# Performance work log

Measured on AMD Instinct MI355X. Metric: run time of the kernel, lower is better.

Reference implementation:

```python
import jax, jax.numpy as jnp
import numpy as np

N, E, D_IN, H, OUT = 50000, 800000, 128, 256, 2
BN_EPS = 1e-5
LN_EPS = 1e-5


def _xavier(k, fi, fo):
    lim = float(np.sqrt(6.0 / (fi + fo)))
    return jax.random.uniform(k, (fi, fo), minval=-lim, maxval=lim, dtype=jnp.float32)


def setup_inputs() -> dict:
    key = jax.random.key(0)
    ks = jax.random.split(key, 8)
    return {
        "x": jax.random.normal(ks[0], (N, D_IN), dtype=jnp.float32),
        "edge_index": jax.random.randint(ks[1], (2, E), 0, N, dtype=jnp.int32),
        "feature_scale": jnp.ones((D_IN,), jnp.float32),
        "feature_bias": jnp.zeros((D_IN,), jnp.float32),
        "bn0_g": jnp.ones((D_IN,), jnp.float32),
        "bn0_b": jnp.zeros((D_IN,), jnp.float32),
        "W1": _xavier(ks[2], D_IN, H), "b1": jnp.zeros((H,), jnp.float32),
        "bn1_g": jnp.ones((H,), jnp.float32), "bn1_b": jnp.zeros((H,), jnp.float32),
        "ln1_g": jnp.ones((H,), jnp.float32), "ln1_b": jnp.zeros((H,), jnp.float32),
        "W2": _xavier(ks[3], H, H), "b2": jnp.zeros((H,), jnp.float32),
        "bn2_g": jnp.ones((H,), jnp.float32), "bn2_b": jnp.zeros((H,), jnp.float32),
        "ln2_g": jnp.ones((H,), jnp.float32), "ln2_b": jnp.zeros((H,), jnp.float32),
        "Wout": _xavier(ks[4], H, OUT), "bout": jnp.zeros((OUT,), jnp.float32),
    }


def _batchnorm(x, g, b):
    # training-mode BatchNorm1d: batch stats over node axis, biased variance
    mu = jnp.mean(x, axis=0)
    var = jnp.mean(jnp.square(x - mu), axis=0)
    return g * (x - mu) * jax.lax.rsqrt(var + BN_EPS) + b


def _layernorm(x, g, b):
    mu = jnp.mean(x, axis=-1, keepdims=True)
    var = jnp.mean(jnp.square(x - mu), axis=-1, keepdims=True)
    return g * (x - mu) * jax.lax.rsqrt(var + LN_EPS) + b


def _gcn(x, W, b, src, dst, dinv):
    # PyG GCNConv with self-loops: D^{-1/2}(A+I)D^{-1/2} X W + b
    h = x @ W                                   # [N, F]
    norm = (dinv[src] * dinv[dst])[:, None]     # [E, 1]
    msg = h[src] * norm                         # [E, F] (dominant traffic)
    agg = jax.ops.segment_sum(msg, dst, num_segments=N)
    return agg + (dinv * dinv)[:, None] * h + b


def _forward(x, feature_scale, feature_bias, bn0_g, bn0_b,
             W1, b1, bn1_g, bn1_b, ln1_g, ln1_b,
             W2, b2, bn2_g, bn2_b, ln2_g, ln2_b,
             Wout, bout, edge_index):
    src, dst = edge_index[0], edge_index[1]
    deg = jax.ops.segment_sum(jnp.ones((E,), x.dtype), dst, num_segments=N) + 1.0
    dinv = jax.lax.rsqrt(deg)

    h = x * feature_scale + feature_bias
    h = _batchnorm(h, bn0_g, bn0_b)            # input_bn; dropout = identity (eval)

    # layer 0 (no residual: i == 0)
    h1 = _gcn(h, W1, b1, src, dst, dinv)
    h1 = jax.nn.relu(h1)
    h1 = _batchnorm(h1, bn1_g, bn1_b)
    h1 = _layernorm(h1, ln1_g, ln1_b)

    # layer 1 (residual add, shapes match)
    h2 = _gcn(h1, W2, b2, src, dst, dinv)
    h2 = jax.nn.relu(h2)
    h2 = _batchnorm(h2, bn2_g, bn2_b)
    h2 = _layernorm(h2, ln2_g, ln2_b)
    h2 = h2 + h1

    return h2 @ Wout + bout


def reference(x, edge_index, feature_scale, feature_bias, bn0_g, bn0_b,
              W1, b1, bn1_g, bn1_b, ln1_g, ln1_b,
              W2, b2, bn2_g, bn2_b, ln2_g, ln2_b,
              Wout, bout):
    return _forward(x, feature_scale, feature_bias, bn0_g, bn0_b,
                    W1, b1, bn1_g, bn1_b, ln1_g, ln1_b,
                    W2, b2, bn2_g, bn2_b, ln2_g, ln2_b,
                    Wout, bout, edge_index)
```

## Files before the change

kernel.cpp:

```cpp
#include <hip/hip_runtime.h>
#include <hip/hip_bf16.h>
#include <stdint.h>

#define N_NODES 50000
#define N_EDGES 800000
#define D_IN    128
#define H_DIM   256
#define BN_EPS  1e-5f
#define LN_EPS  1e-5f
#define NBLK2 782
#define SLICE_ELEMS ((size_t)N_NODES * 32)
#define EDGE_CHUNK 4096
#define BN0_BLOCKS 256
#define PREPX_BLOCKS 6250
#define TR_BLOCKS 256
#define NBKT 196
#define CHUNK 2048
#define RCHUNKS 391

typedef float v4f __attribute__((ext_vector_type(4)));
typedef float v2f __attribute__((ext_vector_type(2)));
typedef short v8s __attribute__((ext_vector_type(8)));
typedef unsigned v4u __attribute__((ext_vector_type(4)));

__device__ __forceinline__ float bflo(unsigned u){ return __uint_as_float(u << 16); }
__device__ __forceinline__ float bfhi(unsigned u){ return __uint_as_float(u & 0xffff0000u); }
__device__ __forceinline__ unsigned short f2bf(float f){
  unsigned u = __float_as_uint(f);
  u += 0x7fffu + ((u >> 16) & 1u);
  return (unsigned short)(u >> 16);
}
__device__ __forceinline__ unsigned pack2(float a, float b){
  return (unsigned)f2bf(a) | ((unsigned)f2bf(b) << 16);
}

__device__ __forceinline__ int block_excl_scan(int v){
  int t = threadIdx.x;
  int lane = t & 63, w = t >> 6;
  int inc = v;
  #pragma unroll
  for (int m = 1; m < 64; m <<= 1){
    int o = __shfl_up(inc, m, 64);
    if (lane >= m) inc += o;
  }
  __shared__ int wsum[4];
  if (lane == 63) wsum[w] = inc;
  __syncthreads();
  int base = 0;
  #pragma unroll
  for (int j = 0; j < 4; ++j) if (j < w) base += wsum[j];
  return base + inc - v;
}

__global__ __launch_bounds__(256) void bn0r1_k(const int* ei, const float* x,
                                               const float* fs, const float* fb,
                                               float* S, float* Q, int* ghist){
  int b = blockIdx.x, t = threadIdx.x;
  if (b >= BN0_BLOCKS){
    __shared__ int lh[NBKT];
    int b2 = b - BN0_BLOCKS;
    for (int i = t; i < NBKT; i += 256) lh[i] = 0;
    __syncthreads();
    int e0 = b2 * CHUNK;
    int n = min(CHUNK, N_EDGES - e0);
    for (int i = t; i < n; i += 256)
      atomicAdd(&lh[ei[N_EDGES + e0 + i] >> 8], 1);
    __syncthreads();
    if (t < NBKT && lh[t] > 0) atomicAdd(&ghist[t], lh[t]);
    return;
  }
  int cl = t & 31, rg = t >> 5;
  int c = cl * 4;
  float4 fs4 = *(const float4*)(fs + c);
  float4 fb4 = *(const float4*)(fb + c);
  float s0=0,s1=0,s2=0,s3=0,q0=0,q1=0,q2=0,q3=0;
  for (int row = b * 8 + rg; row < N_NODES; row += BN0_BLOCKS * 8){
    float4 xv = *(const float4*)(x + (size_t)row * D_IN + c);
    float v0 = xv.x * fs4.x + fb4.x;
    float v1 = xv.y * fs4.y + fb4.y;
    float v2 = xv.z * fs4.z + fb4.z;
    float v3 = xv.w * fs4.w + fb4.w;
    s0 += v0; s1 += v1; s2 += v2; s3 += v3;
    q0 += v0*v0; q1 += v1*v1; q2 += v2*v2; q3 += v3*v3;
  }
  __shared__ float red[256][8];
  red[t][0]=s0; red[t][1]=s1; red[t][2]=s2; red[t][3]=s3;
  red[t][4]=q0; red[t][5]=q1; red[t][6]=q2; red[t][7]=q3;
  __syncthreads();
  float* Sr = S + (b & 3) * D_IN;
  float* Qr = Q + (b & 3) * D_IN;
  if (t < 32){
    float a[8];
    #pragma unroll
    for (int i = 0; i < 8; ++i) a[i] = red[t][i];
    for (int j = 1; j < 8; ++j)
      #pragma unroll
      for (int i = 0; i < 8; ++i) a[i] += red[t + 32*j][i];
    #pragma unroll
    for (int i = 0; i < 4; ++i){ atomicAdd(&Sr[t*4+i], a[i]); atomicAdd(&Qr[t*4+i], a[4+i]); }
  }
}

__global__ __launch_bounds__(256) void r3_k(const int* ei, const int* ghist, int* gcursor, unsigned* ebuf){
  __shared__ unsigned short dstS[CHUNK];
  __shared__ int lh[NBKT], cb[NBKT], sbb[NBKT];
  int t = threadIdx.x;
  int v = (t < NBKT) ? ghist[t] : 0;
  int epre = block_excl_scan(v);
  if (t < NBKT){ sbb[t] = epre; lh[t] = 0; }
  __syncthreads();
  int e0 = blockIdx.x * CHUNK;
  int n = min(CHUNK, N_EDGES - e0);
  for (int i = t; i < n; i += 256){
    int d = ei[N_EDGES + e0 + i];
    dstS[i] = (unsigned short)d;
    atomicAdd(&lh[d >> 8], 1);
  }
  __syncthreads();
  if (t < NBKT && lh[t] > 0) cb[t] = sbb[t] + atomicAdd(&gcursor[t], lh[t]);
  __syncthreads();
  if (t < NBKT) lh[t] = 0;
  __syncthreads();
  for (int i = t; i < n; i += 256){
    int d = dstS[i];
    int bkt = d >> 8;
    int r = atomicAdd(&lh[bkt], 1);
    unsigned src = (unsigned)ei[e0 + i];
    ebuf[cb[bkt] + r] = ((unsigned)(d & 255) << 16) | src;
  }
}

__global__ __launch_bounds__(256) void dloc_k(const unsigned* ebuf, const int* ghist,
                                              int* perm, int* rank, int* offs, float* dinv){
  __shared__ int h[256], dh[128], ep_s[128], W_s[128], lc[128], sbb[NBKT + 1];
  int t = threadIdx.x, b = blockIdx.x;
  int gv = (t < NBKT) ? ghist[t] : 0;
  int gpre = block_excl_scan(gv);
  if (t < NBKT) sbb[t] = gpre;
  if (t == NBKT - 1) sbb[NBKT] = gpre + gv;
  h[t] = 0;
  if (t < 128){ dh[t] = 0; lc[t] = 0; }
  __syncthreads();
  int lo = sbb[b], hi = sbb[b + 1];
  for (int i = lo + t; i < hi; i += 256)
    atomicAdd(&h[(ebuf[i] >> 16) & 255], 1);
  __syncthreads();
  int node = b * 256 + t;
  bool valid = node < N_NODES;
  int deg = valid ? h[t] : 0;
  if (valid) atomicAdd(&dh[min(deg, 127)], 1);
  __syncthreads();
  int cv = (t < 128) ? dh[t] : 0;
  int e1 = block_excl_scan(cv);
  __syncthreads();
  int e2 = block_excl_scan((t < 128) ? cv * t : 0);
  __syncthreads();
  if (t < 128){ ep_s[t] = e1; W_s[t] = e2; }
  __syncthreads();
  if (valid){
    int bin = min(deg, 127);
    int r = atomicAdd(&lc[bin], 1);
    int pl = ep_s[bin] + r;
    int pos = b * 256 + pl;
    perm[pos] = node;
    rank[node] = pos;
    offs[pos] = lo + W_s[bin] + (pl - ep_s[bin]) * deg;
    dinv[node] = rsqrtf((float)deg + 1.0f);
  }
  if (b == 0 && t == 0) offs[N_NODES] = N_EDGES;
}

__global__ __launch_bounds__(256) void r4bprep_k(const unsigned* ebuf, const int* ghist,
                                                 const int* rank, const int* offs,
                                                 unsigned short* edges,
                                                 const float* x, const float* S, const float* Q,
                                                 const float* fs, const float* fb,
                                                 const float* gg, const float* bb,
                                                 unsigned short* xt,
                                                 const float* W1, const float* W2,
                                                 unsigned short* W1t, unsigned short* W2t){
  __shared__ int curs[256], sbb[NBKT + 1];
  int b = blockIdx.x, t = threadIdx.x;
  if (b < NBKT){
    int v = (t < NBKT) ? ghist[t] : 0;
    int epre = block_excl_scan(v);
    if (t < NBKT) sbb[t] = epre;
    if (t == NBKT - 1) sbb[NBKT] = epre + v;
    int node = b * 256 + t;
    if (node < N_NODES) curs[t] = offs[rank[node]];
    __syncthreads();
    int lo = sbb[b], hi = sbb[b + 1];
    for (int i = lo + t; i < hi; i += 256){
      unsigned u = ebuf[i];
      int l8 = (u >> 16) & 255;
      int pos = atomicAdd(&curs[l8], 1);
      edges[pos] = (unsigned short)(u & 0xffffu);
    }
    return;
  }
  if (b < NBKT + PREPX_BLOCKS){
    int i = (b - NBKT) * 256 + t;
    int row = i >> 5; int c = (i & 31) * 4;
    float4 Sv = *(const float4*)(S + c);
    float4 Qv = *(const float4*)(Q + c);
    #pragma unroll
    for (int rep = 1; rep < 4; ++rep){
      float4 s2 = *(const float4*)(S + rep * D_IN + c);
      float4 q2 = *(const float4*)(Q + rep * D_IN + c);
      Sv.x += s2.x; Sv.y += s2.y; Sv.z += s2.z; Sv.w += s2.w;
      Qv.x += q2.x; Qv.y += q2.y; Qv.z += q2.z; Qv.w += q2.w;
    }
    float4 fs4 = *(const float4*)(fs + c);
    float4 fb4 = *(const float4*)(fb + c);
    float4 gg4 = *(const float4*)(gg + c);
    float4 bb4 = *(const float4*)(bb + c);
    const float invN = 1.0f / N_NODES;
    float mu0 = Sv.x*invN, mu1 = Sv.y*invN, mu2 = Sv.z*invN, mu3 = Sv.w*invN;
    float r0 = rsqrtf(Qv.x*invN - mu0*mu0 + BN_EPS);
    float r1 = rsqrtf(Qv.y*invN - mu1*mu1 + BN_EPS);
    float r2 = rsqrtf(Qv.z*invN - mu2*mu2 + BN_EPS);
    float r3 = rsqrtf(Qv.w*invN - mu3*mu3 + BN_EPS);
    float a0 = gg4.x*r0*fs4.x, c0 = gg4.x*r0*(fb4.x - mu0) + bb4.x;
    float a1 = gg4.y*r1*fs4.y, c1 = gg4.y*r1*(fb4.y - mu1) + bb4.y;
    float a2 = gg4.z*r2*fs4.z, c2 = gg4.z*r2*(fb4.z - mu2) + bb4.z;
    float a3 = gg4.w*r3*fs4.w, c3 = gg4.w*r3*(fb4.w - mu3) + bb4.w;
    float4 xv = *(const float4*)(x + (size_t)row * D_IN + c);
    uint2 o;
    o.x = pack2(a0 * xv.x + c0, a1 * xv.y + c1);
    o.y = pack2(a2 * xv.z + c2, a3 * xv.w + c3);
    *(uint2*)(xt + (size_t)row * D_IN + c) = o;
    return;
  }
  int i = (b - NBKT - PREPX_BLOCKS) * 256 + t;
  if (i < D_IN * H_DIM){
    int r = i / H_DIM, c = i % H_DIM;
    W1t[c * D_IN + r] = f2bf(W1[i]);
  }
  if (i < H_DIM * H_DIM){
    int r = i / H_DIM, c = i % H_DIM;
    W2t[c * H_DIM + r] = f2bf(W2[i]);
  }
}

template<int K>
__global__ __launch_bounds__(256) void gemm_k(const unsigned short* A, const unsigned short* Bt,
                                              const float* dinv, unsigned short* C, int M){
  __shared__ __align__(16) short smem[16896];
  __shared__ float dvs[64];
  short* As = smem;
  short* Bs = smem + 64 * 40;
  int t = threadIdx.x;
  int m0 = blockIdx.x * 64;
  int lane = t & 63;
  int w = t >> 6;
  int fr = lane & 15, quad = lane >> 4;
  if (t < 64) dvs[t] = (m0 + t < M) ? dinv[m0 + t] : 0.0f;
  v4f acc[4][4] = {};
  int sr = t >> 2;
  int sk = (t & 3) << 3;
  for (int k0 = 0; k0 < K; k0 += 32){
    __syncthreads();
    uint4 av = {0,0,0,0};
    int arow = m0 + sr;
    if (arow < M) av = *(const uint4*)(A + (size_t)arow * K + k0 + sk);
    *(uint4*)(&As[sr * 40 + sk]) = av;
    #pragma unroll
    for (int j = 0; j < 4; ++j){
      int brow = sr + 64 * j;
      uint4 bv = *(const uint4*)(Bt + (size_t)brow * K + k0 + sk);
      *(uint4*)(&Bs[brow * 40 + sk]) = bv;
    }
    __syncthreads();
    v8s af[4], bf[4];
    #pragma unroll
    for (int mi = 0; mi < 4; ++mi)
      af[mi] = *(const v8s*)(&As[(mi * 16 + fr) * 40 + quad * 8]);
    #pragma unroll
    for (int ni = 0; ni < 4; ++ni)
      bf[ni] = *(const v8s*)(&Bs[(w * 64 + ni * 16 + fr) * 40 + quad * 8]);
    #pragma unroll
    for (int mi = 0; mi < 4; ++mi)
      #pragma unroll
      for (int ni = 0; ni < 4; ++ni)
        acc[mi][ni] = __builtin_amdgcn_mfma_f32_16x16x32_bf16(af[mi], bf[ni], acc[mi][ni], 0, 0, 0);
  }
  __syncthreads();
  short* Cs = smem;
  #pragma unroll
  for (int mi = 0; mi < 4; ++mi)
    #pragma unroll
    for (int ni = 0; ni < 4; ++ni)
      #pragma unroll
      for (int r = 0; r < 4; ++r){
        int row = mi * 16 + quad * 4 + r;
        int col = w * 64 + ni * 16 + fr;
        Cs[row * 264 + col] = (short)f2bf(acc[mi][ni][r] * dvs[row]);
      }
  __syncthreads();
  int orow = t >> 2;
  int grow = m0 + orow;
  if (grow < M){
    #pragma unroll
    for (int j = 0; j < 4; ++j){
      int oc = (t & 3) * 16 + 64 * j;
      v8s v0 = *(const v8s*)(&Cs[orow * 264 + oc]);
      v8s v1 = *(const v8s*)(&Cs[orow * 264 + oc + 8]);
      *(v8s*)(&C[(size_t)(oc >> 5) * SLICE_ELEMS + (size_t)grow * 32 + (oc & 31)]) = v0;
      int oc1 = oc + 8;
      *(v8s*)(&C[(size_t)(oc1 >> 5) * SLICE_ELEMS + (size_t)grow * 32 + (oc1 & 31)]) = v1;
    }
  }
}

#define ACCP(u, A) { v2f d_ = {bflo(u), bfhi(u)}; A += d_; }
#define ACC8(vv) ACCP(vv.x, A0) ACCP(vv.y, A1) ACCP(vv.z, A2) ACCP(vv.w, A3)

__global__ __launch_bounds__(256, 4) void agg_k(const unsigned short* hs, const int* offsets,
                                                const unsigned short* edges, const int* perm,
                                                const float* dinv, const float* bias,
                                                unsigned short* g, float* pS, float* pQ){
  __shared__ unsigned eds32[EDGE_CHUNK / 2];
  __shared__ float wps[4][4][16];
  int t = threadIdx.x;
  int lane = t & 63;
  int wv = t >> 6;
  int slice = blockIdx.x & 7;
  int l4 = lane & 3;
  int grp = blockIdx.x >> 3;
  int nb = grp * 64;
  int idx = nb + (t >> 2);
  int lastn = min(nb + 64, N_NODES);
  int blk0 = offsets[nb];
  int base = blk0 & ~1;
  int blkN = offsets[lastn];
  const unsigned* gsrc = (const unsigned*)(edges + base);
  int nu = min((blkN - base + 1) >> 1, EDGE_CHUNK / 2);
  for (int i = t; i < nu; i += 256)
    eds32[i] = gsrc[i];
  __syncthreads();
  bool act = idx < N_NODES;
  int node = act ? perm[idx] : 0;
  float dvv = act ? dinv[node] : 0.f;
  const uint4* hb4 = (const uint4*)(hs + (size_t)slice * SLICE_ELEMS);
  float4 bb0 = *(const float4*)(bias + slice * 32 + l4 * 8);
  float4 bb1 = *(const float4*)(bias + slice * 32 + l4 * 8 + 4);
  uint4 sv = hb4[(size_t)node * 4 + l4];
  v2f A0 = {bflo(sv.x), bfhi(sv.x)};
  v2f A1 = {bflo(sv.y), bfhi(sv.y)};
  v2f A2 = {bflo(sv.z), bfhi(sv.z)};
  v2f A3 = {bflo(sv.w), bfhi(sv.w)};
  int e  = act ? offsets[idx] : 0;
  int e1 = act ? offsets[idx + 1] : 0;
  if ((e & 1) && e < e1){
    int ru = (e - base) >> 1;
    unsigned d = (ru < EDGE_CHUNK / 2) ? eds32[ru] : gsrc[ru];
    uint4 vv = hb4[(size_t)(d >> 16) * 4 + l4];
    ACC8(vv);
    ++e;
  }
  for (; e + 16 <= e1; e += 16){
    int ru = (e - base) >> 1;
    unsigned dd[8];
    if (ru + 8 <= EDGE_CHUNK / 2){
      #pragma unroll
      for (int j = 0; j < 8; ++j) dd[j] = eds32[ru + j];
    } else {
      #pragma unroll
      for (int j = 0; j < 8; ++j) dd[j] = gsrc[ru + j];
    }
    uint4 v[16];
    #pragma unroll
    for (int j = 0; j < 8; ++j){
      v[2*j]   = hb4[(size_t)(dd[j] & 0xffffu) * 4 + l4];
      v[2*j+1] = hb4[(size_t)(dd[j] >> 16)     * 4 + l4];
    }
    #pragma unroll
    for (int j = 0; j < 16; ++j){ ACC8(v[j]); }
  }
  if (e + 8 <= e1){
    int ru = (e - base) >> 1;
    unsigned dd[4];
    if (ru + 4 <= EDGE_CHUNK / 2){
      #pragma unroll
      for (int j = 0; j < 4; ++j) dd[j] = eds32[ru + j];
    } else {
      #pragma unroll
      for (int j = 0; j < 4; ++j) dd[j] = gsrc[ru + j];
    }
    uint4 v[8];
    #pragma unroll
    for (int j = 0; j < 4; ++j){
      v[2*j]   = hb4[(size_t)(dd[j] & 0xffffu) * 4 + l4];
      v[2*j+1] = hb4[(size_t)(dd[j] >> 16)     * 4 + l4];
    }
    #pragma unroll
    for (int j = 0; j < 8; ++j){ ACC8(v[j]); }
    e += 8;
  }
  if (e + 4 <= e1){
    int ru = (e - base) >> 1;
    unsigned dd[2];
    if (ru + 2 <= EDGE_CHUNK / 2){
      dd[0] = eds32[ru]; dd[1] = eds32[ru + 1];
    } else {
      dd[0] = gsrc[ru]; dd[1] = gsrc[ru + 1];
    }
    uint4 v[4];
    #pragma unroll
    for (int j = 0; j < 2; ++j){
      v[2*j]   = hb4[(size_t)(dd[j] & 0xffffu) * 4 + l4];
      v[2*j+1] = hb4[(size_t)(dd[j] >> 16)     * 4 + l4];
    }
    #pragma unroll
    for (int j = 0; j < 4; ++j){ ACC8(v[j]); }
    e += 4;
  }
  for (; e < e1; ++e){
    int r = e - base;
    unsigned d = ((r >> 1) < EDGE_CHUNK / 2) ? eds32[r >> 1] : gsrc[r >> 1];
    unsigned s = (r & 1) ? (d >> 16) : (d & 0xffffu);
    uint4 vv = hb4[(size_t)s * 4 + l4];
    ACC8(vv);
  }
  float y0 = act ? fmaxf(dvv * A0.x + bb0.x, 0.f) : 0.f;
  float y1 = act ? fmaxf(dvv * A0.y + bb0.y, 0.f) : 0.f;
  float y2 = act ? fmaxf(dvv * A1.x + bb0.z, 0.f) : 0.f;
  float y3 = act ? fmaxf(dvv * A1.y + bb0.w, 0.f) : 0.f;
  float y4 = act ? fmaxf(dvv * A2.x + bb1.x, 0.f) : 0.f;
  float y5 = act ? fmaxf(dvv * A2.y + bb1.y, 0.f) : 0.f;
  float y6 = act ? fmaxf(dvv * A3.x + bb1.z, 0.f) : 0.f;
  float y7 = act ? fmaxf(dvv * A3.y + bb1.w, 0.f) : 0.f;
  if (act){
    v4u o;
    o.x = pack2(y0, y1); o.y = pack2(y2, y3);
    o.z = pack2(y4, y5); o.w = pack2(y6, y7);
    __builtin_nontemporal_store(o, (v4u*)(g + (size_t)node * H_DIM + slice * 32 + l4 * 8));
  }
  float q0 = y0*y0, q1 = y1*y1, q2 = y2*y2, q3 = y3*y3;
  float q4 = y4*y4, q5 = y5*y5, q6 = y6*y6, q7 = y7*y7;
  #pragma unroll
  for (int m = 4; m < 64; m <<= 1){
    y0 += __shfl_xor(y0, m, 64); y1 += __shfl_xor(y1, m, 64);
    y2 += __shfl_xor(y2, m, 64); y3 += __shfl_xor(y3, m, 64);
    y4 += __shfl_xor(y4, m, 64); y5 += __shfl_xor(y5, m, 64);
    y6 += __shfl_xor(y6, m, 64); y7 += __shfl_xor(y7, m, 64);
    q0 += __shfl_xor(q0, m, 64); q1 += __shfl_xor(q1, m, 64);
    q2 += __shfl_xor(q2, m, 64); q3 += __shfl_xor(q3, m, 64);
    q4 += __shfl_xor(q4, m, 64); q5 += __shfl_xor(q5, m, 64);
    q6 += __shfl_xor(q6, m, 64); q7 += __shfl_xor(q7, m, 64);
  }
  if (lane < 4){
    wps[wv][lane][0] = y0; wps[wv][lane][1] = y1; wps[wv][lane][2] = y2; wps[wv][lane][3] = y3;
    wps[wv][lane][4] = y4; wps[wv][lane][5] = y5; wps[wv][lane][6] = y6; wps[wv][lane][7] = y7;
    wps[wv][lane][8] = q0; wps[wv][lane][9] = q1; wps[wv][lane][10] = q2; wps[wv][lane][11] = q3;
    wps[wv][lane][12] = q4; wps[wv][lane][13] = q5; wps[wv][lane][14] = q6; wps[wv][lane][15] = q7;
  }
  __syncthreads();
  if (t < 64){
    int tl = t >> 4, ti = t & 15;
    float v = wps[0][tl][ti] + wps[1][tl][ti] + wps[2][tl][ti] + wps[3][tl][ti];
    int col32 = tl * 8 + (ti & 7);
    if (ti < 8) pS[(size_t)blockIdx.x * 32 + col32] = v;
    else        pQ[(size_t)blockIdx.x * 32 + col32] = v;
  }
}

__global__ __launch_bounds__(1024) void redu_k(const float* pS, const float* pQ,
                                               const float* gg, const float* bb,
                                               float* sc, float* sh){
  __shared__ float ls[32][32], lq[32][32];
  int t = threadIdx.x;
  int slice = blockIdx.x;
  int grp = t >> 5, c32 = t & 31;
  float as = 0.f, aq = 0.f;
  for (int blk2 = grp; blk2 < NBLK2; blk2 += 32){
    size_t o = ((size_t)blk2 * 8 + slice) * 32 + c32;
    as += pS[o]; aq += pQ[o];
  }
  ls[grp][c32] = as; lq[grp][c32] = aq;
  __syncthreads();
  if (t < 32){
    float S = 0.f, Q = 0.f;
    #pragma unroll
    for (int gI = 0; gI < 32; ++gI){ S += ls[gI][t]; Q += lq[gI][t]; }
    int col = slice * 32 + t;
    const float invN = 1.0f / N_NODES;
    float mu = S * invN;
    float rs = rsqrtf(Q * invN - mu * mu + BN_EPS);
    float s = gg[col] * rs;
    sc[col] = s;
    sh[col] = bb[col] - s * mu;
  }
}

__global__ __launch_bounds__(256) void apply1_k(const unsigned short* g, const float* sc, const float* sh,
                                                const float* lng, const float* lnb, unsigned short* h1){
  int t = threadIdx.x;
  int lane32 = t & 31;
  int row = blockIdx.x * 8 + (t >> 5);
  if (row >= N_NODES) return;
  int c = lane32 * 8;
  float4 s40 = *(const float4*)(sc + c);
  float4 s41 = *(const float4*)(sc + c + 4);
  float4 h40 = *(const float4*)(sh + c);
  float4 h41 = *(const float4*)(sh + c + 4);
  uint4 u = *(const uint4*)(g + (size_t)row * H_DIM + c);
  float v0 = s40.x * bflo(u.x) + h40.x;
  float v1 = s40.y * bfhi(u.x) + h40.y;
  float v2 = s40.z * bflo(u.y) + h40.z;
  float v3 = s40.w * bfhi(u.y) + h40.w;
  float v4 = s41.x * bflo(u.z) + h41.x;
  float v5 = s41.y * bfhi(u.z) + h41.y;
  float v6 = s41.z * bflo(u.w) + h41.z;
  float v7 = s41.w * bfhi(u.w) + h41.w;
  float sum = v0+v1+v2+v3+v4+v5+v6+v7;
  float sq  = v0*v0+v1*v1+v2*v2+v3*v3+v4*v4+v5*v5+v6*v6+v7*v7;
  #pragma unroll
  for (int m = 1; m < 32; m <<= 1){ sum += __shfl_xor(sum, m, 64); sq += __shfl_xor(sq, m, 64); }
  float mu = sum * (1.0f / H_DIM);
  float var = sq * (1.0f / H_DIM) - mu * mu;
  float rs = rsqrtf(var + LN_EPS);
  float4 g40 = *(const float4*)(lng + c);
  float4 g41 = *(const float4*)(lng + c + 4);
  float4 b40 = *(const float4*)(lnb + c);
  float4 b41 = *(const float4*)(lnb + c + 4);
  uint4 o;
  o.x = pack2(g40.x * (v0 - mu) * rs + b40.x, g40.y * (v1 - mu) * rs + b40.y);
  o.y = pack2(g40.z * (v2 - mu) * rs + b40.z, g40.w * (v3 - mu) * rs + b40.w);
  o.z = pack2(g41.x * (v4 - mu) * rs + b41.x, g41.y * (v5 - mu) * rs + b41.y);
  o.w = pack2(g41.z * (v6 - mu) * rs + b41.z, g41.w * (v7 - mu) * rs + b41.w);
  *(uint4*)(h1 + (size_t)row * H_DIM + c) = o;
}

__global__ __launch_bounds__(256) void apply2_k(const unsigned short* g, const float* sc, const float* sh,
                                                const float* lng, const float* lnb,
                                                const unsigned short* h1, const float* Wout,
                                                const float* bout, float* out){
  int t = threadIdx.x;
  int lane32 = t & 31;
  int row = blockIdx.x * 8 + (t >> 5);
  if (row >= N_NODES) return;
  int c = lane32 * 8;
  float4 s40 = *(const float4*)(sc + c);
  float4 s41 = *(const float4*)(sc + c + 4);
  float4 h40 = *(const float4*)(sh + c);
  float4 h41 = *(const float4*)(sh + c + 4);
  uint4 u = *(const uint4*)(g + (size_t)row * H_DIM + c);
  float v0 = s40.x * bflo(u.x) + h40.x;
  float v1 = s40.y * bfhi(u.x) + h40.y;
  float v2 = s40.z * bflo(u.y) + h40.z;
  float v3 = s40.w * bfhi(u.y) + h40.w;
  float v4 = s41.x * bflo(u.z) + h41.x;
  float v5 = s41.y * bfhi(u.z) + h41.y;
  float v6 = s41.z * bflo(u.w) + h41.z;
  float v7 = s41.w * bfhi(u.w) + h41.w;
  float sum = v0+v1+v2+v3+v4+v5+v6+v7;
  float sq  = v0*v0+v1*v1+v2*v2+v3*v3+v4*v4+v5*v5+v6*v6+v7*v7;
  #pragma unroll
  for (int m = 1; m < 32; m <<= 1){ sum += __shfl_xor(sum, m, 64); sq += __shfl_xor(sq, m, 64); }
  float mu = sum * (1.0f / H_DIM);
  float var = sq * (1.0f / H_DIM) - mu * mu;
  float rs = rsqrtf(var + LN_EPS);
  float4 g40 = *(const float4*)(lng + c);
  float4 g41 = *(const float4*)(lng + c + 4);
  float4 b40 = *(const float4*)(lnb + c);
  float4 b41 = *(const float4*)(lnb + c + 4);
  uint4 hr = *(const uint4*)(h1 + (size_t)row * H_DIM + c);
  float y0 = g40.x * (v0 - mu) * rs + b40.x + bflo(hr.x);
  float y1 = g40.y * (v1 - mu) * rs + b40.y + bfhi(hr.x);
  float y2 = g40.z * (v2 - mu) * rs + b40.z + bflo(hr.y);
  float y3 = g40.w * (v3 - mu) * rs + b40.w + bfhi(hr.y);
  float y4 = g41.x * (v4 - mu) * rs + b41.x + bflo(hr.z);
  float y5 = g41.y * (v5 - mu) * rs + b41.y + bfhi(hr.z);
  float y6 = g41.z * (v6 - mu) * rs + b41.z + bflo(hr.w);
  float y7 = g41.w * (v7 - mu) * rs + b41.w + bfhi(hr.w);
  float4 w0 = *(const float4*)(Wout + c * 2);
  float4 w1 = *(const float4*)(Wout + c * 2 + 4);
  float4 w2 = *(const float4*)(Wout + c * 2 + 8);
  float4 w3 = *(const float4*)(Wout + c * 2 + 12);
  float o0 = y0*w0.x + y1*w0.z + y2*w1.x + y3*w1.z + y4*w2.x + y5*w2.z + y6*w3.x + y7*w3.z;
  float o1 = y0*w0.y + y1*w0.w + y2*w1.y + y3*w1.w + y4*w2.y + y5*w2.w + y6*w3.y + y7*w3.w;
  #pragma unroll
  for (int m = 1; m < 32; m <<= 1){ o0 += __shfl_xor(o0, m, 64); o1 += __shfl_xor(o1, m, 64); }
  if (lane32 == 0){
    out[(size_t)row * 2 + 0] = o0 + bout[0];
    out[(size_t)row * 2 + 1] = o1 + bout[1];
  }
}

extern "C" void kernel_launch(void* const* d_in, const int* in_sizes, int n_in,
                              void* d_out, int out_size, void* d_ws, size_t ws_size,
                              hipStream_t stream) {
  const float* x    = (const float*)d_in[0];
  const int*   ei   = (const int*)d_in[1];
  const float* fs   = (const float*)d_in[2];
  const float* fb   = (const float*)d_in[3];
  const float* bn0g = (const float*)d_in[4];
  const float* bn0b = (const float*)d_in[5];
  const float* W1   = (const float*)d_in[6];
  const float* b1   = (const float*)d_in[7];
  const float* bn1g = (const float*)d_in[8];
  const float* bn1b = (const float*)d_in[9];
  const float* ln1g = (const float*)d_in[10];
  const float* ln1b = (const float*)d_in[11];
  const float* W2   = (const float*)d_in[12];
  const float* b2   = (const float*)d_in[13];
  const float* bn2g = (const float*)d_in[14];
  const float* bn2b = (const float*)d_in[15];
  const float* ln2g = (const float*)d_in[16];
  const float* ln2b = (const float*)d_in[17];
  const float* Wout = (const float*)d_in[18];
  const float* bout = (const float*)d_in[19];
  float* out = (float*)d_out;

  char* w = (char*)d_ws;
  float* bn0S  = (float*)(w + 0);
  float* bn0Q  = (float*)(w + 2048);
  int*   ghist  = (int*)(w + 5120);
  int*   gcursor= (int*)(w + 5904);
  const size_t ZERO_BYTES = 6688;
  float* sc1   = (float*)(w + 7488);
  float* sh1   = (float*)(w + 8512);
  float* sc2   = (float*)(w + 9536);
  float* sh2   = (float*)(w + 10560);
  float* dinv  = (float*)(w + 211584);
  int*   offs  = (int*)(w + 411584);
  int*   perm  = (int*)(w + 611712);
  int*   rank  = (int*)(w + 811712);
  unsigned short* edges = (unsigned short*)(w + 1011712);
  unsigned short* xt   = (unsigned short*)(w + 2611712);
  unsigned short* W1t  = (unsigned short*)(w + 15411712);
  unsigned short* W2t  = (unsigned short*)(w + 15477248);
  unsigned short* hlin = (unsigned short*)(w + 15608320);
  unsigned*       ebuf = (unsigned*)(w + 15608320);
  unsigned short* gbuf = (unsigned short*)(w + 41208320);
  unsigned short* h1   = (unsigned short*)(w + 66808320);
  float* pS    = (float*)(w + 92408320);
  float* pQ    = (float*)(w + 94008832);

  (void)in_sizes; (void)n_in; (void)out_size; (void)ws_size;

  hipMemsetAsync(d_ws, 0, ZERO_BYTES, stream);

  bn0r1_k<<<BN0_BLOCKS + RCHUNKS, 256, 0, stream>>>(ei, x, fs, fb, bn0S, bn0Q, ghist);
  r3_k<<<RCHUNKS, 256, 0, stream>>>(ei, ghist, gcursor, ebuf);
  dloc_k<<<NBKT, 256, 0, stream>>>(ebuf, ghist, perm, rank, offs, dinv);
  r4bprep_k<<<NBKT + PREPX_BLOCKS + TR_BLOCKS, 256, 0, stream>>>(
      ebuf, ghist, rank, offs, edges, x, bn0S, bn0Q, fs, fb, bn0g, bn0b, xt, W1, W2, W1t, W2t);

  int ggrid = (N_NODES + 63) / 64;
  int agg_blocks = NBLK2 * 8;

  gemm_k<D_IN><<<ggrid, 256, 0, stream>>>(xt, W1t, dinv, hlin, N_NODES);
  agg_k<<<agg_blocks, 256, 0, stream>>>(hlin, offs, edges, perm, dinv, b1, gbuf, pS, pQ);
  redu_k<<<8, 1024, 0, stream>>>(pS, pQ, bn1g, bn1b, sc1, sh1);
  apply1_k<<<(N_NODES + 7) / 8, 256, 0, stream>>>(gbuf, sc1, sh1, ln1g, ln1b, h1);

  gemm_k<H_DIM><<<ggrid, 256, 0, stream>>>(h1, W2t, dinv, hlin, N_NODES);
  agg_k<<<agg_blocks, 256, 0, stream>>>(hlin, offs, edges, perm, dinv, b2, gbuf, pS, pQ);
  redu_k<<<8, 1024, 0, stream>>>(pS, pQ, bn2g, bn2b, sc2, sh2);
  apply2_k<<<(N_NODES + 7) / 8, 256, 0, stream>>>(gbuf, sc2, sh2, ln2g, ln2b, h1, Wout, bout, out);
}
```

Baseline: 340.7 us.

## Fuse degree-local sort into edge scatter kernel, drop LDS edge staging in aggregation

Merges the per-bucket degree sort (dloc_k) into the edge-scatter/prep kernel so each bucket block computes degrees, permutation and offsets and then scatters edges itself. This removes one kernel launch and the rank array round trip. The aggregation kernel no longer stages each block's edge list into shared memory and reads packed edge indices directly from global memory, which drops a syncthreads and the LDS fill at the cost of more global loads. BN0 statistic blocks are raised from 256 to 1024, with 8 atomic replica rows instead of 4 to spread contention.

```diff
diff --git a/kernel.cpp b/kernel.cpp
--- a/kernel.cpp
+++ b/kernel.cpp
@@ -10,8 +10,7 @@
 #define LN_EPS  1e-5f
 #define NBLK2 782
 #define SLICE_ELEMS ((size_t)N_NODES * 32)
-#define EDGE_CHUNK 4096
-#define BN0_BLOCKS 256
+#define BN0_BLOCKS 1024
 #define PREPX_BLOCKS 6250
 #define TR_BLOCKS 256
 #define NBKT 196
@@ -87,8 +86,8 @@
   red[t][0]=s0; red[t][1]=s1; red[t][2]=s2; red[t][3]=s3;
   red[t][4]=q0; red[t][5]=q1; red[t][6]=q2; red[t][7]=q3;
   __syncthreads();
-  float* Sr = S + (b & 3) * D_IN;
-  float* Qr = Q + (b & 3) * D_IN;
+  float* Sr = S + (b & 7) * D_IN;
+  float* Qr = Q + (b & 7) * D_IN;
   if (t < 32){
     float a[8];
     #pragma unroll
@@ -130,72 +129,60 @@
   }
 }
 
-__global__ __launch_bounds__(256) void dloc_k(const unsigned* ebuf, const int* ghist,
-                                              int* perm, int* rank, int* offs, float* dinv){
-  __shared__ int h[256], dh[128], ep_s[128], W_s[128], lc[128], sbb[NBKT + 1];
-  int t = threadIdx.x, b = blockIdx.x;
-  int gv = (t < NBKT) ? ghist[t] : 0;
-  int gpre = block_excl_scan(gv);
-  if (t < NBKT) sbb[t] = gpre;
-  if (t == NBKT - 1) sbb[NBKT] = gpre + gv;
-  h[t] = 0;
-  if (t < 128){ dh[t] = 0; lc[t] = 0; }
-  __syncthreads();
-  int lo = sbb[b], hi = sbb[b + 1];
-  for (int i = lo + t; i < hi; i += 256)
-    atomicAdd(&h[(ebuf[i] >> 16) & 255], 1);
-  __syncthreads();
-  int node = b * 256 + t;
-  bool valid = node < N_NODES;
-  int deg = valid ? h[t] : 0;
-  if (valid) atomicAdd(&dh[min(deg, 127)], 1);
-  __syncthreads();
-  int cv = (t < 128) ? dh[t] : 0;
-  int e1 = block_excl_scan(cv);
-  __syncthreads();
-  int e2 = block_excl_scan((t < 128) ? cv * t : 0);
-  __syncthreads();
-  if (t < 128){ ep_s[t] = e1; W_s[t] = e2; }
-  __syncthreads();
-  if (valid){
-    int bin = min(deg, 127);
-    int r = atomicAdd(&lc[bin], 1);
-    int pl = ep_s[bin] + r;
-    int pos = b * 256 + pl;
-    perm[pos] = node;
-    rank[node] = pos;
-    offs[pos] = lo + W_s[bin] + (pl - ep_s[bin]) * deg;
-    dinv[node] = rsqrtf((float)deg + 1.0f);
-  }
-  if (b == 0 && t == 0) offs[N_NODES] = N_EDGES;
-}
-
-__global__ __launch_bounds__(256) void r4bprep_k(const unsigned* ebuf, const int* ghist,
-                                                 const int* rank, const int* offs,
-                                                 unsigned short* edges,
-                                                 const float* x, const float* S, const float* Q,
-                                                 const float* fs, const float* fb,
-                                                 const float* gg, const float* bb,
-                                                 unsigned short* xt,
-                                                 const float* W1, const float* W2,
-                                                 unsigned short* W1t, unsigned short* W2t){
-  __shared__ int curs[256], sbb[NBKT + 1];
+__global__ __launch_bounds__(256) void sortprep_k(const unsigned* ebuf, const int* ghist,
+                                                  int* perm, int* offs, float* dinv,
+                                                  unsigned short* edges,
+                                                  const float* x, const float* S, const float* Q,
+                                                  const float* fs, const float* fb,
+                                                  const float* gg, const float* bb,
+                                                  unsigned short* xt,
+                                                  const float* W1, const float* W2,
+                                                  unsigned short* W1t, unsigned short* W2t){
   int b = blockIdx.x, t = threadIdx.x;
   if (b < NBKT){
-    int v = (t < NBKT) ? ghist[t] : 0;
-    int epre = block_excl_scan(v);
-    if (t < NBKT) sbb[t] = epre;
-    if (t == NBKT - 1) sbb[NBKT] = epre + v;
+    __shared__ int h[256], dh[128], ep_s[128], W_s[128], lc[128], curs[256], sbb[NBKT + 1];
+    int gv = (t < NBKT) ? ghist[t] : 0;
+    int gpre = block_excl_scan(gv);
+    if (t < NBKT) sbb[t] = gpre;
+    if (t == NBKT - 1) sbb[NBKT] = gpre + gv;
+    h[t] = 0;
+    if (t < 128){ dh[t] = 0; lc[t] = 0; }
+    __syncthreads();
+    int lo = sbb[b], hi = sbb[b + 1];
+    for (int i = lo + t; i < hi; i += 256)
+      atomicAdd(&h[(ebuf[i] >> 16) & 255], 1);
+    __syncthreads();
     int node = b * 256 + t;
-    if (node < N_NODES) curs[t] = offs[rank[node]];
-    __syncthreads();
-    int lo = sbb[b], hi = sbb[b + 1];
+    bool valid = node < N_NODES;
+    int deg = valid ? h[t] : 0;
+    if (valid) atomicAdd(&dh[min(deg, 127)], 1);
+    __syncthreads();
+    int cv = (t < 128) ? dh[t] : 0;
+    int e1 = block_excl_scan(cv);
+    __syncthreads();
+    int e2 = block_excl_scan((t < 128) ? cv * t : 0);
+    __syncthreads();
+    if (t < 128){ ep_s[t] = e1; W_s[t] = e2; }
+    __syncthreads();
+    if (valid){
+      int bin = min(deg, 127);
+      int r = atomicAdd(&lc[bin], 1);
+      int pl = ep_s[bin] + r;
+      int pos = b * 256 + pl;
+      int off = lo + W_s[bin] + (pl - ep_s[bin]) * deg;
+      perm[pos] = node;
+      offs[pos] = off;
+      dinv[node] = rsqrtf((float)deg + 1.0f);
+      curs[t] = off;
+    }
+    __syncthreads();
     for (int i = lo + t; i < hi; i += 256){
       unsigned u = ebuf[i];
       int l8 = (u >> 16) & 255;
       int pos = atomicAdd(&curs[l8], 1);
       edges[pos] = (unsigned short)(u & 0xffffu);
     }
+    if (b == 0 && t == 0) offs[N_NODES] = N_EDGES;
     return;
   }
   if (b < NBKT + PREPX_BLOCKS){
@@ -204,7 +191,7 @@
     float4 Sv = *(const float4*)(S + c);
     float4 Qv = *(const float4*)(Q + c);
     #pragma unroll
-    for (int rep = 1; rep < 4; ++rep){
+    for (int rep = 1; rep < 8; ++rep){
       float4 s2 = *(const float4*)(S + rep * D_IN + c);
       float4 q2 = *(const float4*)(Q + rep * D_IN + c);
       Sv.x += s2.x; Sv.y += s2.y; Sv.z += s2.z; Sv.w += s2.w;
@@ -319,7 +306,6 @@
                                                 const unsigned short* edges, const int* perm,
                                                 const float* dinv, const float* bias,
                                                 unsigned short* g, float* pS, float* pQ){
-  __shared__ unsigned eds32[EDGE_CHUNK / 2];
   __shared__ float wps[4][4][16];
   int t = threadIdx.x;
   int lane = t & 63;
@@ -329,19 +315,11 @@
   int grp = blockIdx.x >> 3;
   int nb = grp * 64;
   int idx = nb + (t >> 2);
-  int lastn = min(nb + 64, N_NODES);
-  int blk0 = offsets[nb];
-  int base = blk0 & ~1;
-  int blkN = offsets[lastn];
-  const unsigned* gsrc = (const unsigned*)(edges + base);
-  int nu = min((blkN - base + 1) >> 1, EDGE_CHUNK / 2);
-  for (int i = t; i < nu; i += 256)
-    eds32[i] = gsrc[i];
-  __syncthreads();
   bool act = idx < N_NODES;
   int node = act ? perm[idx] : 0;
   float dvv = act ? dinv[node] : 0.f;
   const uint4* hb4 = (const uint4*)(hs + (size_t)slice * SLICE_ELEMS);
+  const unsigned* ew = (const unsigned*)edges;
   float4 bb0 = *(const float4*)(bias + slice * 32 + l4 * 8);
   float4 bb1 = *(const float4*)(bias + slice * 32 + l4 * 8 + 4);
   uint4 sv = hb4[(size_t)node * 4 + l4];
@@ -352,22 +330,16 @@
   int e  = act ? offsets[idx] : 0;
   int e1 = act ? offsets[idx + 1] : 0;
   if ((e & 1) && e < e1){
-    int ru = (e - base) >> 1;
-    unsigned d = (ru < EDGE_CHUNK / 2) ? eds32[ru] : gsrc[ru];
+    unsigned d = ew[e >> 1];
     uint4 vv = hb4[(size_t)(d >> 16) * 4 + l4];
     ACC8(vv);
     ++e;
   }
   for (; e + 16 <= e1; e += 16){
-    int ru = (e - base) >> 1;
+    int ru = e >> 1;
     unsigned dd[8];
-    if (ru + 8 <= EDGE_CHUNK / 2){
-      #pragma unroll
-      for (int j = 0; j < 8; ++j) dd[j] = eds32[ru + j];
-    } else {
-      #pragma unroll
-      for (int j = 0; j < 8; ++j) dd[j] = gsrc[ru + j];
-    }
+    #pragma unroll
+    for (int j = 0; j < 8; ++j) dd[j] = ew[ru + j];
     uint4 v[16];
     #pragma unroll
     for (int j = 0; j < 8; ++j){
@@ -378,15 +350,10 @@
     for (int j = 0; j < 16; ++j){ ACC8(v[j]); }
   }
   if (e + 8 <= e1){
-    int ru = (e - base) >> 1;
+    int ru = e >> 1;
     unsigned dd[4];
-    if (ru + 4 <= EDGE_CHUNK / 2){
-      #pragma unroll
-      for (int j = 0; j < 4; ++j) dd[j] = eds32[ru + j];
-    } else {
-      #pragma unroll
-      for (int j = 0; j < 4; ++j) dd[j] = gsrc[ru + j];
-    }
+    #pragma unroll
+    for (int j = 0; j < 4; ++j) dd[j] = ew[ru + j];
     uint4 v[8];
     #pragma unroll
     for (int j = 0; j < 4; ++j){
@@ -398,27 +365,20 @@
     e += 8;
   }
   if (e + 4 <= e1){
-    int ru = (e - base) >> 1;
-    unsigned dd[2];
-    if (ru + 2 <= EDGE_CHUNK / 2){
-      dd[0] = eds32[ru]; dd[1] = eds32[ru + 1];
-    } else {
-      dd[0] = gsrc[ru]; dd[1] = gsrc[ru + 1];
-    }
+    int ru = e >> 1;
+    unsigned dd0 = ew[ru], dd1 = ew[ru + 1];
     uint4 v[4];
-    #pragma unroll
-    for (int j = 0; j < 2; ++j){
-      v[2*j]   = hb4[(size_t)(dd[j] & 0xffffu) * 4 + l4];
-      v[2*j+1] = hb4[(size_t)(dd[j] >> 16)     * 4 + l4];
-    }
+    v[0] = hb4[(size_t)(dd0 & 0xffffu) * 4 + l4];
+    v[1] = hb4[(size_t)(dd0 >> 16)     * 4 + l4];
+    v[2] = hb4[(size_t)(dd1 & 0xffffu) * 4 + l4];
+    v[3] = hb4[(size_t)(dd1 >> 16)     * 4 + l4];
     #pragma unroll
     for (int j = 0; j < 4; ++j){ ACC8(v[j]); }
     e += 4;
   }
   for (; e < e1; ++e){
-    int r = e - base;
-    unsigned d = ((r >> 1) < EDGE_CHUNK / 2) ? eds32[r >> 1] : gsrc[r >> 1];
-    unsigned s = (r & 1) ? (d >> 16) : (d & 0xffffu);
+    unsigned d = ew[e >> 1];
+    unsigned s = (e & 1) ? (d >> 16) : (d & 0xffffu);
     uint4 vv = hb4[(size_t)s * 4 + l4];
     ACC8(vv);
   }
@@ -615,18 +575,17 @@
 
   char* w = (char*)d_ws;
   float* bn0S  = (float*)(w + 0);
-  float* bn0Q  = (float*)(w + 2048);
-  int*   ghist  = (int*)(w + 5120);
-  int*   gcursor= (int*)(w + 5904);
-  const size_t ZERO_BYTES = 6688;
-  float* sc1   = (float*)(w + 7488);
-  float* sh1   = (float*)(w + 8512);
-  float* sc2   = (float*)(w + 9536);
-  float* sh2   = (float*)(w + 10560);
+  float* bn0Q  = (float*)(w + 4096);
+  int*   ghist  = (int*)(w + 8192);
+  int*   gcursor= (int*)(w + 8976);
+  const size_t ZERO_BYTES = 9760;
+  float* sc1   = (float*)(w + 10240);
+  float* sh1   = (float*)(w + 11264);
+  float* sc2   = (float*)(w + 12288);
+  float* sh2   = (float*)(w + 13312);
   float* dinv  = (float*)(w + 211584);
   int*   offs  = (int*)(w + 411584);
   int*   perm  = (int*)(w + 611712);
-  int*   rank  = (int*)(w + 811712);
   unsigned short* edges = (unsigned short*)(w + 1011712);
   unsigned short* xt   = (unsigned short*)(w + 2611712);
   unsigned short* W1t  = (unsigned short*)(w + 15411712);
@@ -644,9 +603,8 @@
 
   bn0r1_k<<<BN0_BLOCKS + RCHUNKS, 256, 0, stream>>>(ei, x, fs, fb, bn0S, bn0Q, ghist);
   r3_k<<<RCHUNKS, 256, 0, stream>>>(ei, ghist, gcursor, ebuf);
-  dloc_k<<<NBKT, 256, 0, stream>>>(ebuf, ghist, perm, rank, offs, dinv);
-  r4bprep_k<<<NBKT + PREPX_BLOCKS + TR_BLOCKS, 256, 0, stream>>>(
-      ebuf, ghist, rank, offs, edges, x, bn0S, bn0Q, fs, fb, bn0g, bn0b, xt, W1, W2, W1t, W2t);
+  sortprep_k<<<NBKT + PREPX_BLOCKS + TR_BLOCKS, 256, 0, stream>>>(
+      ebuf, ghist, perm, offs, dinv, edges, x, bn0S, bn0Q, fs, fb, bn0g, bn0b, xt, W1, W2, W1t, W2t);
 
   int ggrid = (N_NODES + 63) / 64;
   int agg_blocks = NBLK2 * 8;
```

New measurement: 344.6 us. Within noise of the previous version (+1.1%).
